# Performance work log

Hardware: AMD Instinct MI355X
Metric: run time of the kernel (lower is better)

Reference implementation:

```python
import jax, jax.numpy as jnp
import numpy as np


def setup_inputs() -> dict:
    key = jax.random.key(0)
    k1, k2, k3 = jax.random.split(key, 3)
    B, C, H, W = 32, 768, 24, 24
    feat1 = jax.random.normal(k1, (B, C, H, W), dtype=jnp.float32)
    feat2 = jax.random.normal(k2, (B, C, H, W), dtype=jnp.float32)
    gamma = jax.random.normal(k3, (1,), dtype=jnp.float32)
    return {"feat1": feat1, "feat2": feat2, "gamma": gamma}


def reference(feat1, feat2, gamma):
    # CMA: channel-wise cross-modal attention over flattened spatial dim.
    B, C, H, W = feat1.shape
    q = feat1.reshape(B, C, H * W)          # [B, C, HW]
    kv = feat2.reshape(B, C, H * W)         # [B, C, HW] (k and v share this)
    attn = jnp.einsum('bcn,bdn->bcd', q, kv)          # [B, C, C] = q @ k^T
    attn = jax.nn.softmax(attn, axis=-1)
    info = jnp.einsum('bcd,bdn->bcn', attn, kv)       # [B, C, HW]
    info = info.reshape(B, C, H, W)
    return gamma[0] * info + feat1
```

## Files before the change

### kernel.cpp

```cpp
#include <hip/hip_runtime.h>

#define B_  32
#define C_  768
#define HW_ 576

#define NCQ 18
#define NCP 24

typedef _Float16 half8 __attribute__((ext_vector_type(8)));
typedef _Float16 half4 __attribute__((ext_vector_type(4)));
typedef float    f32x4 __attribute__((ext_vector_type(4)));

__device__ __forceinline__ void g2l16(const void* g, void* l) {
    __builtin_amdgcn_global_load_lds(
        (const __attribute__((address_space(1))) unsigned int*)g,
        (__attribute__((address_space(3))) unsigned int*)l, 16, 0, 0);
}

#define VM(N) asm volatile("s_waitcnt vmcnt(" #N ")" ::: "memory")


__global__ __launch_bounds__(256) void prep3(const float* __restrict__ f1,
                                             const float* __restrict__ f2,
                                             char* __restrict__ q16,
                                             char* __restrict__ kv16,
                                             char* __restrict__ vt,
                                             int b0, int cur, int nst) {
    __shared__ float Vsh[32 * 201];
    const int bid = blockIdx.x;
    if (bid < nst) {
        const int bz = bid % cur, u = bid / cur;
        const int ti = u >> 2, rg = u & 3;
        const float* s1 = f1 + ((size_t)(b0 + bz) * C_ + ti * 128 + rg * 32) * HW_;
        const float* s2 = f2 + ((size_t)(b0 + bz) * C_ + ti * 128 + rg * 32) * HW_;
        char* dq = q16  + ((size_t)(bz * 6 + ti)) * (NCQ * 8192);
        char* dk = kv16 + ((size_t)(bz * 6 + ti)) * (NCQ * 8192);
        #pragma unroll
        for (int it = 0; it < 18; ++it) {
            int g     = it * 1024 + threadIdx.x * 4;
            int row_l = g / 576;
            int col   = g - row_l * 576;
            int row   = rg * 32 + row_l;
            int k0    = col >> 5, kk = col & 31;
            int x     = (kk >> 3) ^ ((row >> 1) & 3);
            size_t doff = (size_t)k0 * 8192 + row * 64 + x * 16 + (kk & 7) * 2;
            f32x4 v1 = *(const f32x4*)(s1 + g);
            f32x4 v2 = *(const f32x4*)(s2 + g);
            half4 h1, h2;
            #pragma unroll
            for (int e = 0; e < 4; ++e) {
                h1[e] = (_Float16)v1[e];
                h2[e] = (_Float16)v2[e];
            }
            *(half4*)(dq + doff) = h1;
            *(half4*)(dk + doff) = h2;
        }
    } else {
        int bid2 = bid - nst;
        const int bz = bid2 % cur, u = bid2 / cur;
        int k0 = u / 3, tj = u % 3;
        int b  = b0 + bz;
        int t  = threadIdx.x;
        #pragma unroll
        for (int p = 0; p < 6; ++p) {
            int fidx = p * 256 + t;
            int dd = fidx / 48, c4 = fidx % 48;
            f32x4 v = *(const f32x4*)(f2 + ((size_t)b * C_ + k0 * 32 + dd) * HW_ + tj * 192 + c4 * 4);
            #pragma unroll
            for (int e = 0; e < 4; ++e) Vsh[dd * 201 + c4 * 4 + e] = v[e];
        }
        __syncthreads();
        char* ob = vt + ((size_t)(bz * 3 + tj) * NCP + k0) * 12288;
        #pragma unroll
        for (int p = 0; p < 3; ++p) {
            int o = p * 256 + t;
            int x = o & 3, n = o >> 2;
            int kc = x ^ ((n >> 1) & 3);
            half8 h;
            #pragma unroll
            for (int j = 0; j < 8; ++j) h[j] = (_Float16)Vsh[(kc * 8 + j) * 201 + n];
            *(half8*)(ob + o * 16) = h;
        }
    }
}

__global__ __launch_bounds__(512, 4) void qk6(const char* __restrict__ q16,
                                              const char* __restrict__ kv16,
                                              float* __restrict__ attn,
                                              float2* __restrict__ part,
                                              int cur) {
    __shared__ __align__(16) char S[3][24576];
    const int wg = blockIdx.x;
    const int bz = wg % cur, u = wg / cur;
    const int ti = u >> 2, tj = u & 3;
    const int t = threadIdx.x, lane = t & 63, w = t >> 6;
    const int rsub = lane >> 2, cb = (lane & 3) * 16;

    const char *p0, *p1, *p2;
    int o0, o1, o2;
    {
        auto arow = [&](int l) {
            int gr = ti * 192 + 16 * l + rsub;
            return q16 + ((size_t)(bz * 6 + (gr >> 7)) * NCQ) * 8192 + (gr & 127) * 64 + cb;
        };
        auto brow = [&](int l) {
            int gd = tj * 192 + 16 * l + rsub;
            return kv16 + ((size_t)(bz * 6 + (gd >> 7)) * NCQ) * 8192 + (gd & 127) * 64 + cb;
        };
        if (w < 4) {
            p0 = arow(2 * w);     o0 = (2 * w) * 1024;
            p1 = arow(2 * w + 1); o1 = (2 * w + 1) * 1024;
            p2 = brow(8 + w);     o2 = 12288 + (8 + w) * 1024;
        } else {
            int v = w - 4;
            p0 = brow(2 * v);     o0 = 12288 + (2 * v) * 1024;
            p1 = brow(2 * v + 1); o1 = 12288 + (2 * v + 1) * 1024;
            p2 = arow(8 + v);     o2 = (8 + v) * 1024;
        }
    }

    const int wr = (w >> 1) * 48, wc = (w & 1) * 96;
    const int r16 = lane & 15, cg = lane >> 4;
    int offA[3], offB[6];
    #pragma unroll
    for (int m = 0; m < 3; ++m) {
        int ra = wr + m * 16 + r16;
        offA[m] = ra * 64 + ((cg ^ ((ra >> 1) & 3)) << 4);
    }
    #pragma unroll
    for (int n = 0; n < 6; ++n) {
        int rb = wc + n * 16 + r16;
        offB[n] = 12288 + rb * 64 + ((cg ^ ((rb >> 1) & 3)) << 4);
    }

    f32x4 acc[3][6] = {};

#define STG(SLOT) do {                          \
        char* sb_ = &S[SLOT][0];                \
        g2l16(p0, sb_ + o0);                    \
        g2l16(p1, sb_ + o1);                    \
        g2l16(p2, sb_ + o2);                    \
        p0 += 8192; p1 += 8192; p2 += 8192;     \
    } while (0)

    STG(0); STG(1);
    int rd = 0, st = 2;
    for (int c = 0; c < NCQ; ++c) {
        if (c + 2 < NCQ) {
            STG(st); st = (st == 2) ? 0 : st + 1;
            VM(6);
        } else if (c + 2 == NCQ) {
            VM(3);
        } else {
            VM(0);
        }
        __builtin_amdgcn_s_barrier();
        const char* sb = &S[rd][0];
        rd = (rd == 2) ? 0 : rd + 1;
        half8 a0 = *(const half8*)(sb + offA[0]);
        half8 a1 = *(const half8*)(sb + offA[1]);
        half8 a2 = *(const half8*)(sb + offA[2]);
        __builtin_amdgcn_s_setprio(1);
        #pragma unroll
        for (int n = 0; n < 6; ++n) {
            half8 bn = *(const half8*)(sb + offB[n]);
            acc[0][n] = __builtin_amdgcn_mfma_f32_16x16x32_f16(a0, bn, acc[0][n], 0, 0, 0);
            acc[1][n] = __builtin_amdgcn_mfma_f32_16x16x32_f16(a1, bn, acc[1][n], 0, 0, 0);
            acc[2][n] = __builtin_amdgcn_mfma_f32_16x16x32_f16(a2, bn, acc[2][n], 0, 0, 0);
        }
        __builtin_amdgcn_s_setprio(0);
        __builtin_amdgcn_s_barrier();
    }
#undef STG

    const int col = lane & 15, rbase = (lane >> 4) * 4;
    #pragma unroll
    for (int m = 0; m < 3; ++m)
        #pragma unroll
        for (int n = 0; n < 6; ++n)
            #pragma unroll
            for (int rg = 0; rg < 4; ++rg) {
                int grow = ti * 192 + wr + m * 16 + rbase + rg;
                int gcol = tj * 192 + wc + n * 16 + col;
                attn[(((size_t)bz * 6 + (grow >> 7)) * NCP + (gcol >> 5)) * 4096
                     + (grow & 127) * 32 + (gcol & 31)] = acc[m][n][rg];
            }

    const int half = w & 1;
    #pragma unroll
    for (int m = 0; m < 3; ++m)
        #pragma unroll
        for (int rg = 0; rg < 4; ++rg) {
            float mx = -1e30f;
            #pragma unroll
            for (int n = 0; n < 6; ++n) mx = fmaxf(mx, acc[m][n][rg]);
            #pragma unroll
            for (int o = 1; o < 16; o <<= 1) mx = fmaxf(mx, __shfl_xor(mx, o));
            float s = 0.f;
            #pragma unroll
            for (int n = 0; n < 6; ++n) s += __expf(acc[m][n][rg] - mx);
            #pragma unroll
            for (int o = 1; o < 16; o <<= 1) s += __shfl_xor(s, o);
            if ((lane & 15) == 0) {
                int row = wr + m * 16 + (lane >> 4) * 4 + rg;
                part[((size_t)bz * C_ + ti * 192 + row) * 8 + tj * 2 + half] =
                    make_float2(mx, s);
            }
        }
}

__global__ __launch_bounds__(512, 4) void pv10(const float* __restrict__ attn,
                                               const char* __restrict__ vt,
                                               const float2* __restrict__ part,
                                               const float* __restrict__ gamma,
                                               const float* __restrict__ f1,
                                               float* __restrict__ out,
                                               int b0, int cur) {
    __shared__ __align__(16) char S[4][20480];
    const int wg = blockIdx.x;
    const int bz = wg % cur, u = wg / cur;
    const int ti = u / 3, tj = u % 3;
    const int t = threadIdx.x, lane = t & 63, w = t >> 6;
    const int rsub = lane >> 2, cbb = (lane & 3) * 16;

    const int r0 = t >> 2;
    const int g4 = t & 3;
    const float* srcA = attn + (((size_t)bz * 6 + ti) * NCP) * 4096 + t * 8;
    const int aw0 = r0 * 64 + ((g4 ^ ((r0 >> 1) & 3)) << 4);

    float2 ms0;
    {
        const float2* pr = part + ((size_t)bz * C_ + ti * 128 + r0) * 8;
        float2 p8[8];
        #pragma unroll
        for (int i = 0; i < 8; ++i) p8[i] = pr[i];
        float m = p8[0].x;
        #pragma unroll
        for (int i = 1; i < 8; ++i) m = fmaxf(m, p8[i].x);
        float s = 0.f;
        #pragma unroll
        for (int i = 0; i < 8; ++i) s += p8[i].y * __expf(p8[i].x - m);
        ms0 = make_float2(m, gamma[0] / s);
    }

    const char* vbase = vt + ((size_t)(bz * 3 + tj) * NCP) * 12288;
    const char *pB0, *pB1;
    int ob0, ob1;
    if (w < 4) {
        pB0 = vbase + (32 * w + rsub) * 64 + cbb;          ob0 = 8192 + (32 * w) * 64;
        pB1 = vbase + (32 * w + 16 + rsub) * 64 + cbb;     ob1 = 8192 + (32 * w + 16) * 64;
    } else {
        pB0 = vbase + (128 + 16 * (w - 4) + rsub) * 64 + cbb;
        ob0 = 8192 + (128 + 16 * (w - 4)) * 64;
        pB1 = vbase; ob1 = 0;
    }

    const int wr = (w >> 2) * 64, wc = (w & 3) * 48;
    const int r16 = lane & 15, cg = lane >> 4;
    int offA[4], offB[3];
    #pragma unroll
    for (int m = 0; m < 4; ++m) {
        int ra = wr + m * 16 + r16;
        offA[m] = ra * 64 + ((cg ^ ((ra >> 1) & 3)) << 4);
    }
    #pragma unroll
    for (int n = 0; n < 3; ++n) {
        int rb = wc + n * 16 + r16;
        offB[n] = 8192 + rb * 64 + ((cg ^ ((rb >> 1) & 3)) << 4);
    }

    f32x4 acc[4][3] = {};
    f32x4 vaA0, vaA1;
    f32x4 vaB0, vaB1;

#define STG_B(SLOT) do {                                  \
        g2l16(pB0, &S[SLOT][0] + ob0); pB0 += 12288;      \
        if (w < 4) { g2l16(pB1, &S[SLOT][0] + ob1); pB1 += 12288; } \
    } while (0)
#define LD_A(V0, V1) do { V0 = *(const f32x4*)srcA; V1 = *(const f32x4*)(srcA + 4); \
                          srcA += 4096; } while (0)
#define WR_A(SLOT, V0, V1) do {                                        \
        half8 h_;                                                      \
        _Pragma("unroll")                                              \
        for (int e = 0; e < 4; ++e) {                                  \
            h_[e]     = (_Float16)(__expf(V0[e] - ms0.x) * ms0.y);     \
            h_[4 + e] = (_Float16)(__expf(V1[e] - ms0.x) * ms0.y);     \
        }                                                              \
        *(half8*)(&S[SLOT][0] + aw0) = h_;                             \
    } while (0)
#define MFMA_SLOT(SB) do {                                             \
        const char* sb_ = (SB);                                        \
        half8 a_[4], b_[3];                                            \
        _Pragma("unroll")                                              \
        for (int m = 0; m < 4; ++m) a_[m] = *(const half8*)(sb_ + offA[m]); \
        _Pragma("unroll")                                              \
        for (int n = 0; n < 3; ++n) b_[n] = *(const half8*)(sb_ + offB[n]); \
        _Pragma("unroll")                                              \
        for (int m = 0; m < 4; ++m)                                    \
            _Pragma("unroll")                                          \
            for (int n = 0; n < 3; ++n)                                \
                acc[m][n] = __builtin_amdgcn_mfma_f32_16x16x32_f16(a_[m], b_[n], acc[m][n], 0, 0, 0); \
    } while (0)

    LD_A(vaA0, vaA1);
    WR_A(0, vaA0, vaA1);
    LD_A(vaB0, vaB1);
    WR_A(1, vaB0, vaB1);
    STG_B(0); STG_B(1);
    LD_A(vaA0, vaA1);
    LD_A(vaB0, vaB1);

    for (int p = 0; p < 12; ++p) {
        const int sa = (2 * p) & 3;
        asm volatile("s_waitcnt lgkmcnt(0)" ::: "memory");
        __builtin_amdgcn_s_barrier();
        if (p < 11) { STG_B((sa + 2) & 3); STG_B((sa + 3) & 3); }
        if (p < 11) { if (w < 4) VM(8); else VM(6); }
        else        { VM(0); }
        __builtin_amdgcn_s_barrier();

        __builtin_amdgcn_s_setprio(1);
        MFMA_SLOT(&S[sa][0]);
        MFMA_SLOT(&S[sa ^ 1][0]);
        __builtin_amdgcn_s_setprio(0);

        if (p < 11) {
            WR_A((sa + 2) & 3, vaA0, vaA1);
            WR_A((sa + 3) & 3, vaB0, vaB1);
            if (p < 10) {
                LD_A(vaA0, vaA1);
                LD_A(vaB0, vaB1);
            }
        }
    }
#undef MFMA_SLOT
#undef WR_A
#undef LD_A
#undef STG_B

    const int b = b0 + bz;
    const float* f1b = f1 + ((size_t)b * C_ + ti * 128) * HW_ + tj * 192;
    float*       ob  = out + ((size_t)b * C_ + ti * 128) * HW_ + tj * 192;
    const int col = lane & 15, rbase = (lane >> 4) * 4;
    #pragma unroll
    for (int m = 0; m < 4; ++m)
        #pragma unroll
        for (int n = 0; n < 3; ++n)
            #pragma unroll
            for (int rg = 0; rg < 4; ++rg) {
                int r2 = wr + m * 16 + rbase + rg;
                int c2 = wc + n * 16 + col;
                ob[(size_t)r2 * HW_ + c2] = acc[m][n][rg] + f1b[(size_t)r2 * HW_ + c2];
            }
}

extern "C" void kernel_launch(void* const* d_in, const int* in_sizes, int n_in,
                              void* d_out, int out_size, void* d_ws, size_t ws_size,
                              hipStream_t stream) {
    const float* feat1 = (const float*)d_in[0];
    const float* feat2 = (const float*)d_in[1];
    const float* gamma = (const float*)d_in[2];
    float* out = (float*)d_out;

    const size_t SZ_Q    = (size_t)C_ * HW_ * 2;
    const size_t SZ_ATTN = (size_t)C_ * C_  * 4;
    const size_t SZ_PART = (size_t)C_ * 8 * 8;
    const size_t per_batch = SZ_ATTN + 3 * SZ_Q + SZ_PART;

    int nb = (int)(ws_size / per_batch);
    if (nb < 1) nb = 1;
    if (nb > B_) nb = B_;

    char* ws     = (char*)d_ws;
    float* attn  = (float*)ws;
    char* q16    = ws + (size_t)nb * SZ_ATTN;
    char* kv16   = q16 + (size_t)nb * SZ_Q;
    char* vtb    = kv16 + (size_t)nb * SZ_Q;
    float2* part = (float2*)(vtb + (size_t)nb * SZ_Q);

    for (int b0 = 0; b0 < B_; b0 += nb) {
        int cur = (B_ - b0 < nb) ? (B_ - b0) : nb;
        prep3<<<cur * 96, 256, 0, stream>>>(feat1, feat2, q16, kv16, vtb, b0, cur, cur * 24);
        qk6<<<cur * 16, 512, 0, stream>>>(q16, kv16, attn, part, cur);
        pv10<<<cur * 18, 512, 0, stream>>>(attn, vtb, part, gamma, feat1, out, b0, cur);
    }
}
```

Before: 143.0 us.

## Store tile-local exponentiated attention in fp16 and rescale in PV kernel

The QK kernel now exponentiates scores against its tile-local row max and writes them as fp16 instead of raw fp32 logits, halving the attention intermediate's global traffic and workspace. The PV kernel loads half8 directly and applies a per-column-tile correction factor exp(m_tile - m_row)*gamma/sum instead of computing exp per element. The vmcnt waits are adjusted for fewer loads, and the main loop is fully unrolled so the tile index folds to constants. Storing unnormalized exponentials in fp16 may lose some precision relative to the fp32 logits.

```diff
diff --git a/kernel.cpp b/kernel.cpp
--- a/kernel.cpp
+++ b/kernel.cpp
@@ -86,7 +86,7 @@
 
 __global__ __launch_bounds__(512, 4) void qk6(const char* __restrict__ q16,
                                               const char* __restrict__ kv16,
-                                              float* __restrict__ attn,
+                                              _Float16* __restrict__ attnE,
                                               float2* __restrict__ part,
                                               int cur) {
     __shared__ __align__(16) char S[3][24576];
@@ -173,20 +173,8 @@
     }
 #undef STG
 
-    const int col = lane & 15, rbase = (lane >> 4) * 4;
-    #pragma unroll
-    for (int m = 0; m < 3; ++m)
-        #pragma unroll
-        for (int n = 0; n < 6; ++n)
-            #pragma unroll
-            for (int rg = 0; rg < 4; ++rg) {
-                int grow = ti * 192 + wr + m * 16 + rbase + rg;
-                int gcol = tj * 192 + wc + n * 16 + col;
-                attn[(((size_t)bz * 6 + (grow >> 7)) * NCP + (gcol >> 5)) * 4096
-                     + (grow & 127) * 32 + (gcol & 31)] = acc[m][n][rg];
-            }
-
     const int half = w & 1;
+    float mxv[3][4];
     #pragma unroll
     for (int m = 0; m < 3; ++m)
         #pragma unroll
@@ -196,6 +184,7 @@
             for (int n = 0; n < 6; ++n) mx = fmaxf(mx, acc[m][n][rg]);
             #pragma unroll
             for (int o = 1; o < 16; o <<= 1) mx = fmaxf(mx, __shfl_xor(mx, o));
+            mxv[m][rg] = mx;
             float s = 0.f;
             #pragma unroll
             for (int n = 0; n < 6; ++n) s += __expf(acc[m][n][rg] - mx);
@@ -207,9 +196,23 @@
                     make_float2(mx, s);
             }
         }
-}
-
-__global__ __launch_bounds__(512, 4) void pv10(const float* __restrict__ attn,
+
+    const int col = lane & 15, rbase = (lane >> 4) * 4;
+    #pragma unroll
+    for (int m = 0; m < 3; ++m)
+        #pragma unroll
+        for (int n = 0; n < 6; ++n)
+            #pragma unroll
+            for (int rg = 0; rg < 4; ++rg) {
+                int grow = ti * 192 + wr + m * 16 + rbase + rg;
+                int gcol = tj * 192 + wc + n * 16 + col;
+                attnE[(((size_t)bz * 6 + (grow >> 7)) * NCP + (gcol >> 5)) * 4096
+                      + (grow & 127) * 32 + (gcol & 31)] =
+                    (_Float16)__expf(acc[m][n][rg] - mxv[m][rg]);
+            }
+}
+
+__global__ __launch_bounds__(512, 4) void pv11(const _Float16* __restrict__ attnE,
                                                const char* __restrict__ vt,
                                                const float2* __restrict__ part,
                                                const float* __restrict__ gamma,
@@ -225,22 +228,23 @@
 
     const int r0 = t >> 2;
     const int g4 = t & 3;
-    const float* srcA = attn + (((size_t)bz * 6 + ti) * NCP) * 4096 + t * 8;
+    const char* srcA = (const char*)(attnE + (((size_t)bz * 6 + ti) * NCP) * 4096) + t * 16;
     const int aw0 = r0 * 64 + ((g4 ^ ((r0 >> 1) & 3)) << 4);
 
-    float2 ms0;
+    float2 pm[8];
+    float m_row, inv;
     {
         const float2* pr = part + ((size_t)bz * C_ + ti * 128 + r0) * 8;
-        float2 p8[8];
-        #pragma unroll
-        for (int i = 0; i < 8; ++i) p8[i] = pr[i];
-        float m = p8[0].x;
-        #pragma unroll
-        for (int i = 1; i < 8; ++i) m = fmaxf(m, p8[i].x);
+        #pragma unroll
+        for (int i = 0; i < 8; ++i) pm[i] = pr[i];
+        float m = pm[0].x;
+        #pragma unroll
+        for (int i = 1; i < 8; ++i) m = fmaxf(m, pm[i].x);
         float s = 0.f;
         #pragma unroll
-        for (int i = 0; i < 8; ++i) s += p8[i].y * __expf(p8[i].x - m);
-        ms0 = make_float2(m, gamma[0] / s);
+        for (int i = 0; i < 8; ++i) s += pm[i].y * __expf(pm[i].x - m);
+        m_row = m;
+        inv = gamma[0] / s;
     }
 
     const char* vbase = vt + ((size_t)(bz * 3 + tj) * NCP) * 12288;
@@ -270,22 +274,19 @@
     }
 
     f32x4 acc[4][3] = {};
-    f32x4 vaA0, vaA1;
-    f32x4 vaB0, vaB1;
+    half8 vaA, vaB;
 
 #define STG_B(SLOT) do {                                  \
         g2l16(pB0, &S[SLOT][0] + ob0); pB0 += 12288;      \
         if (w < 4) { g2l16(pB1, &S[SLOT][0] + ob1); pB1 += 12288; } \
     } while (0)
-#define LD_A(V0, V1) do { V0 = *(const f32x4*)srcA; V1 = *(const f32x4*)(srcA + 4); \
-                          srcA += 4096; } while (0)
-#define WR_A(SLOT, V0, V1) do {                                        \
+#define LD_A(V) do { V = *(const half8*)srcA; srcA += 8192; } while (0)
+#define WR_A(SLOT, V, H) do {                                          \
+        const float fac_ = __expf(pm[H].x - m_row) * inv;              \
         half8 h_;                                                      \
         _Pragma("unroll")                                              \
-        for (int e = 0; e < 4; ++e) {                                  \
-            h_[e]     = (_Float16)(__expf(V0[e] - ms0.x) * ms0.y);     \
-            h_[4 + e] = (_Float16)(__expf(V1[e] - ms0.x) * ms0.y);     \
-        }                                                              \
+        for (int e = 0; e < 8; ++e)                                    \
+            h_[e] = (_Float16)((float)V[e] * fac_);                    \
         *(half8*)(&S[SLOT][0] + aw0) = h_;                             \
     } while (0)
 #define MFMA_SLOT(SB) do {                                             \
@@ -302,20 +303,21 @@
                 acc[m][n] = __builtin_amdgcn_mfma_f32_16x16x32_f16(a_[m], b_[n], acc[m][n], 0, 0, 0); \
     } while (0)
 
-    LD_A(vaA0, vaA1);
-    WR_A(0, vaA0, vaA1);
-    LD_A(vaB0, vaB1);
-    WR_A(1, vaB0, vaB1);
+    LD_A(vaA);
+    WR_A(0, vaA, 0);
+    LD_A(vaB);
+    WR_A(1, vaB, 0);
     STG_B(0); STG_B(1);
-    LD_A(vaA0, vaA1);
-    LD_A(vaB0, vaB1);
-
+    LD_A(vaA);
+    LD_A(vaB);
+
+    #pragma unroll
     for (int p = 0; p < 12; ++p) {
         const int sa = (2 * p) & 3;
         asm volatile("s_waitcnt lgkmcnt(0)" ::: "memory");
         __builtin_amdgcn_s_barrier();
         if (p < 11) { STG_B((sa + 2) & 3); STG_B((sa + 3) & 3); }
-        if (p < 11) { if (w < 4) VM(8); else VM(6); }
+        if (p < 11) { if (w < 4) VM(6); else VM(4); }
         else        { VM(0); }
         __builtin_amdgcn_s_barrier();
 
@@ -325,11 +327,11 @@
         __builtin_amdgcn_s_setprio(0);
 
         if (p < 11) {
-            WR_A((sa + 2) & 3, vaA0, vaA1);
-            WR_A((sa + 3) & 3, vaB0, vaB1);
+            WR_A((sa + 2) & 3, vaA, (2 * p + 2) / 3);
+            WR_A((sa + 3) & 3, vaB, (2 * p + 3) / 3);
             if (p < 10) {
-                LD_A(vaA0, vaA1);
-                LD_A(vaB0, vaB1);
+                LD_A(vaA);
+                LD_A(vaB);
             }
         }
     }
@@ -363,7 +365,7 @@
     float* out = (float*)d_out;
 
     const size_t SZ_Q    = (size_t)C_ * HW_ * 2;
-    const size_t SZ_ATTN = (size_t)C_ * C_  * 4;
+    const size_t SZ_ATTN = (size_t)C_ * C_  * 2;
     const size_t SZ_PART = (size_t)C_ * 8 * 8;
     const size_t per_batch = SZ_ATTN + 3 * SZ_Q + SZ_PART;
 
@@ -371,17 +373,17 @@
     if (nb < 1) nb = 1;
     if (nb > B_) nb = B_;
 
-    char* ws     = (char*)d_ws;
-    float* attn  = (float*)ws;
-    char* q16    = ws + (size_t)nb * SZ_ATTN;
-    char* kv16   = q16 + (size_t)nb * SZ_Q;
-    char* vtb    = kv16 + (size_t)nb * SZ_Q;
-    float2* part = (float2*)(vtb + (size_t)nb * SZ_Q);
+    char* ws        = (char*)d_ws;
+    _Float16* attnE = (_Float16*)ws;
+    char* q16       = ws + (size_t)nb * SZ_ATTN;
+    char* kv16      = q16 + (size_t)nb * SZ_Q;
+    char* vtb       = kv16 + (size_t)nb * SZ_Q;
+    float2* part    = (float2*)(vtb + (size_t)nb * SZ_Q);
 
     for (int b0 = 0; b0 < B_; b0 += nb) {
         int cur = (B_ - b0 < nb) ? (B_ - b0) : nb;
         prep3<<<cur * 96, 256, 0, stream>>>(feat1, feat2, q16, kv16, vtb, b0, cur, cur * 24);
-        qk6<<<cur * 16, 512, 0, stream>>>(q16, kv16, attn, part, cur);
-        pv10<<<cur * 18, 512, 0, stream>>>(attn, vtb, part, gamma, feat1, out, b0, cur);
-    }
-}
+        qk6<<<cur * 16, 512, 0, stream>>>(q16, kv16, attnE, part, cur);
+        pv11<<<cur * 18, 512, 0, stream>>>(attnE, vtb, part, gamma, feat1, out, b0, cur);
+    }
+}
```

New measurement: 127.4 us. 10.9% less time.
